# Kernel tuning notes

Measured on AMD Instinct MI355X. Metric: run time of the kernel, lower is better.

## Reference

```python
import jax, jax.numpy as jnp
import numpy as np
import math

L = 4          # n_layers
H = 8          # n_heads
TOP_K = 32
Z99 = 2.326347874040841
SQRT2PI = math.sqrt(2.0 * math.pi)
CONF = 0.99
SCALE_MAX = 1.0  # model not calibrated -> _scale_max = 1.0
EPS = 1e-5


def layer_norm(x, g, b):
    m = jnp.mean(x, axis=-1, keepdims=True)
    v = jnp.var(x, axis=-1, keepdims=True)
    return (x - m) * jax.lax.rsqrt(v + EPS) * g + b


def pos_encoding(T, D):
    pos = jnp.arange(T, dtype=jnp.float32)[:, None]
    div = jnp.exp(jnp.arange(0, D, 2, dtype=jnp.float32) * (-math.log(10000.0) / D))
    pe = jnp.zeros((T, D), jnp.float32)
    pe = pe.at[:, 0::2].set(jnp.sin(pos * div))
    pe = pe.at[:, 1::2].set(jnp.cos(pos * div))
    return pe  # [T, D]


def sparse_attn(h, Wq, Wk, Wv, Wo, bo):
    B, T, D = h.shape
    dh = D // H
    q = (h @ Wq).reshape(B, T, H, dh)
    k = (h @ Wk).reshape(B, T, H, dh)
    v = (h @ Wv).reshape(B, T, H, dh)
    scores = jnp.einsum('bthd,bshd->bhts', q, k) / np.float32(np.sqrt(dh))  # [B,H,T,T]
    kth = jax.lax.top_k(scores, TOP_K)[0][..., -1:]  # k-th largest per row
    scores = jnp.where(scores < kth, -jnp.inf, scores)
    attn = jax.nn.softmax(scores, axis=-1)
    attn = jnp.nan_to_num(attn)
    out = jnp.einsum('bhts,bshd->bthd', attn, v).reshape(B, T, D)
    return out @ Wo + bo


def encoder_layer(h, Wq, Wk, Wv, Wo, bo, W1, b1, W2, b2, g1, be1, g2, be2):
    h = layer_norm(h + sparse_attn(h, Wq, Wk, Wv, Wo, bo), g1, be1)
    ff = jax.nn.gelu((h @ W1) + b1, approximate=False) @ W2 + b2
    return layer_norm(h + ff, g2, be2)


def setup_inputs() -> dict:
    key = jax.random.key(0)
    B, T, Din, D, Dff = 16, 1024, 64, 512, 2048
    ks = jax.random.split(key, 12)

    def p(k, shape):
        return jax.random.normal(k, shape, jnp.float32) * np.float32(1.0 / np.sqrt(shape[-2]))

    return {
        'x': jax.random.normal(ks[0], (B, T, Din), jnp.float32),
        'W_in': p(ks[1], (Din, D)), 'b_in': jnp.zeros((D,), jnp.float32),
        'Wq': p(ks[2], (L, D, D)), 'Wk': p(ks[3], (L, D, D)),
        'Wv': p(ks[4], (L, D, D)), 'Wo': p(ks[5], (L, D, D)),
        'bo': jnp.zeros((L, D), jnp.float32),
        'W1': p(ks[6], (L, D, Dff)), 'b1': jnp.zeros((L, Dff), jnp.float32),
        'W2': p(ks[7], (L, Dff, D)), 'b2': jnp.zeros((L, D), jnp.float32),
        'g1': jnp.ones((L, D), jnp.float32), 'be1': jnp.zeros((L, D), jnp.float32),
        'g2': jnp.ones((L, D), jnp.float32), 'be2': jnp.zeros((L, D), jnp.float32),
        'gm': jnp.ones((D,), jnp.float32), 'bm': jnp.zeros((D,), jnp.float32),
        'Wm': p(ks[8], (D, 1)), 'cm': jnp.zeros((1,), jnp.float32),
        'gs': jnp.ones((D,), jnp.float32), 'bs': jnp.zeros((D,), jnp.float32),
        'Ws': p(ks[9], (D, 1)), 'cs': jnp.zeros((1,), jnp.float32),
    }


def reference(x, W_in, b_in, Wq, Wk, Wv, Wo, bo, W1, b1, W2, b2, g1, be1, g2, be2,
              gm, bm, Wm, cm, gs, bs, Ws, cs):
    B, T, _ = x.shape
    D = W_in.shape[1]
    h = (x @ W_in) + b_in + pos_encoding(T, D)[None]  # input_proj + pos enc (dropout=eval)
    for i in range(L):
        h = encoder_layer(h, Wq[i], Wk[i], Wv[i], Wo[i], bo[i],
                          W1[i], b1[i], W2[i], b2[i], g1[i], be1[i], g2[i], be2[i])
    h_last = h[:, -1, :]  # [B, D]
    mu = (layer_norm(h_last, gm, bm) @ Wm + cm)[:, 0]
    scale = jax.nn.sigmoid(layer_norm(h_last, gs, bs) @ Ws + cs)[:, 0] * SCALE_MAX
    var_pred = mu + scale * Z99
    phi_z = math.exp(-0.5 * Z99 ** 2) / SQRT2PI
    es_pred = mu + scale * phi_z / (1.0 - CONF)
    return jnp.stack([mu, scale, var_pred, es_pred])  # [4, B]
```

## Files before the change

### kernel.cpp

```cpp
#include <hip/hip_runtime.h>
#include <math.h>


typedef unsigned int u32;
typedef __attribute__((ext_vector_type(8))) _Float16 f16x8;
typedef __attribute__((ext_vector_type(4))) float f32x4;

__device__ __forceinline__ void g2l16(const void* g, void* l) {
  __builtin_amdgcn_global_load_lds(
      (const __attribute__((address_space(1))) u32*)g,
      (__attribute__((address_space(3))) u32*)l, 16, 0, 0);
}

__global__ __launch_bounds__(256) void wprep_kernel(const float* __restrict__ src,
    unsigned short* __restrict__ dst_hi, unsigned short* __restrict__ dst_lo,
    int K, int N) {
  __shared__ float t[64][65];
  src    += (size_t)blockIdx.z * K * N;
  dst_hi += (size_t)blockIdx.z * K * N;
  dst_lo += (size_t)blockIdx.z * K * N;
  const int k0 = blockIdx.y * 64, n0 = blockIdx.x * 64;
#pragma unroll
  for (int i = 0; i < 16; i++) {
    int idx = threadIdx.x + i * 256;
    int kk = idx >> 6, nn = idx & 63;
    t[kk][nn] = src[(size_t)(k0 + kk) * N + n0 + nn];
  }
  __syncthreads();
#pragma unroll
  for (int i = 0; i < 16; i++) {
    int idx = threadIdx.x + i * 256;
    int nn = idx >> 6, kk = idx & 63;
    float w = t[kk][nn];
    _Float16 hi = (_Float16)w;
    _Float16 lo = (_Float16)(w - (float)hi);
    union { _Float16 h; unsigned short u; } a, b; a.h = hi; b.h = lo;
    dst_hi[(size_t)(n0 + nn) * K + k0 + kk] = a.u;
    dst_lo[(size_t)(n0 + nn) * K + k0 + kk] = b.u;
  }
}

__global__ __launch_bounds__(256) void gemm_split(const float* __restrict__ A,
    const unsigned short* __restrict__ Bhi, const unsigned short* __restrict__ Blo,
    const float* __restrict__ bias, float* __restrict__ C,
    int M, int N, int K, int ldb, int epi) {
  __shared__ float          As[128 * 64];
  __shared__ unsigned short BsH[128 * 64];
  __shared__ unsigned short BsL[128 * 64];
  const int tid = threadIdx.x;
  const int w = tid >> 6, l = tid & 63;
  const int wm = w >> 1, wn = w & 1;
  const int bm = blockIdx.y * 128, bn = blockIdx.x * 128;
  f32x4 acc[4][4] = {};

  for (int k0 = 0; k0 < K; k0 += 64) {
    if (k0) __syncthreads();
#pragma unroll
    for (int i = 0; i < 8; i++) {
      int cl = i * 256 + w * 64 + l;
      int row = cl >> 4, c = cl & 15;
      int col = (((c >> 1) ^ (row & 7)) * 8) + (c & 1) * 4;
      g2l16(A + (size_t)(bm + row) * K + k0 + col, As + (size_t)(i * 256 + w * 64) * 4);
    }
#pragma unroll
    for (int i = 0; i < 4; i++) {
      int cl = i * 256 + w * 64 + l;
      int row = cl >> 3, c = cl & 7;
      int col = ((c ^ (row & 7)) * 8);
      size_t src = (size_t)(bn + row) * ldb + k0 + col;
      g2l16(Bhi + src, BsH + (size_t)(i * 256 + w * 64) * 8);
      g2l16(Blo + src, BsL + (size_t)(i * 256 + w * 64) * 8);
    }
    __syncthreads();
#pragma unroll
    for (int kk = 0; kk < 2; kk++) {
      f16x8 ahi[4], alo[4], bhi[4], blo[4];
      const int c16 = kk * 4 + (l >> 4);
#pragma unroll
      for (int i = 0; i < 4; i++) {
        int ar = wm * 64 + i * 16 + (l & 15);
        const float* ap = &As[ar * 64 + ((c16 ^ (ar & 7)) * 8)];
        float4 a0 = *(const float4*)ap;
        float4 a1 = *(const float4*)(ap + 4);
        float av[8] = {a0.x, a0.y, a0.z, a0.w, a1.x, a1.y, a1.z, a1.w};
#pragma unroll
        for (int e = 0; e < 8; e++) {
          _Float16 hh = (_Float16)av[e];
          ahi[i][e] = hh;
          alo[i][e] = (_Float16)(av[e] - (float)hh);
        }
        int br = wn * 64 + i * 16 + (l & 15);
        bhi[i] = *(const f16x8*)&BsH[br * 64 + ((c16 ^ (br & 7)) * 8)];
        blo[i] = *(const f16x8*)&BsL[br * 64 + ((c16 ^ (br & 7)) * 8)];
      }
#pragma unroll
      for (int i = 0; i < 4; i++)
#pragma unroll
        for (int j = 0; j < 4; j++) {
          acc[i][j] = __builtin_amdgcn_mfma_f32_16x16x32_f16(ahi[i], bhi[j], acc[i][j], 0, 0, 0);
          acc[i][j] = __builtin_amdgcn_mfma_f32_16x16x32_f16(alo[i], bhi[j], acc[i][j], 0, 0, 0);
          acc[i][j] = __builtin_amdgcn_mfma_f32_16x16x32_f16(ahi[i], blo[j], acc[i][j], 0, 0, 0);
        }
    }
  }

  float bj[4], fr[4];
#pragma unroll
  for (int j = 0; j < 4; j++) {
    int col = bn + wn * 64 + j * 16 + (l & 15);
    bj[j] = (bias != nullptr) ? bias[col] : 0.f;
    fr[j] = (epi == 3) ? __expf((float)(col & ~1) * (-9.210340371976184f / 512.0f)) : 0.f;
  }
#pragma unroll
  for (int i = 0; i < 4; i++) {
#pragma unroll
    for (int e = 0; e < 4; e++) {
      int row = bm + wm * 64 + i * 16 + (l >> 4) * 4 + e;
#pragma unroll
      for (int j = 0; j < 4; j++) {
        int col = bn + wn * 64 + j * 16 + (l & 15);
        float v = acc[i][j][e] + bj[j];
        if (epi == 2) v = 0.5f * v * (1.0f + erff(v * 0.70710678118654752f));
        if (epi == 3) {
          float ang = (float)(row & 1023) * fr[j];
          v += (col & 1) ? cosf(ang) : sinf(ang);
        }
        if (epi == 4) v += C[(size_t)row * N + col];
        C[(size_t)row * N + col] = v;
      }
    }
  }
}

__device__ __forceinline__ unsigned f2o(float f) {
  unsigned b = __float_as_uint(f);
  return (b & 0x80000000u) ? ~b : (b | 0x80000000u);
}
__device__ __forceinline__ float o2f(unsigned u) {
  unsigned b = (u & 0x80000000u) ? (u & 0x7fffffffu) : ~u;
  return __uint_as_float(b);
}

__global__ __launch_bounds__(512, 4) void attn_kernel(float* __restrict__ qa,
    const float* __restrict__ ka, const float* __restrict__ va) {
  __shared__ __align__(16) float smem[16384 + 2048];
  float* ktile = smem;
  float* qlds  = smem + 16384;
  float* cval  = smem;
  int*   cidx  = (int*)smem + 32 * 96;

  const int tid = threadIdx.x;
  const int wave = tid >> 6, lane = tid & 63;
  const int bh = blockIdx.y, b = bh >> 3, hh = bh & 7;
  const int t0 = blockIdx.x * 32;
  const float* kb = ka + (size_t)b * 1024 * 512 + hh * 64;
  const float* vb = va + (size_t)b * 1024 * 512 + hh * 64;

  {
    int row = tid >> 4, qq = tid & 15;
    float4 qv = *(const float4*)(qa + ((size_t)(b * 1024 + t0 + row)) * 512 + hh * 64 + qq * 4);
    qv.x *= 0.125f; qv.y *= 0.125f; qv.z *= 0.125f; qv.w *= 0.125f;
    *(float4*)(qlds + row * 64 + qq * 4) = qv;
  }

  float sc[4][16] = {};

#pragma unroll
  for (int tile = 0; tile < 4; ++tile) {
    const float* kg = kb + (size_t)tile * 256 * 512;
#pragma unroll
    for (int i = 0; i < 8; ++i) {
      int idx = tid + i * 512;
      int row = idx >> 4, qq = idx & 15;
      float4 kv = *(const float4*)(kg + (size_t)row * 512 + qq * 4);
      *(float4*)(ktile + row * 64 + ((qq ^ (row & 7)) * 4)) = kv;
    }
    __syncthreads();
#pragma unroll 4
    for (int dq = 0; dq < 16; ++dq) {
      float4 qr[4];
#pragma unroll
      for (int r = 0; r < 4; ++r)
        qr[r] = *(const float4*)(qlds + (wave * 4 + r) * 64 + dq * 4);
      const int swz = (dq ^ (lane & 7)) * 4;
#pragma unroll
      for (int j = 0; j < 4; ++j) {
        float4 kv = *(const float4*)(ktile + (j * 64 + lane) * 64 + swz);
#pragma unroll
        for (int r = 0; r < 4; ++r) {
          float a = sc[r][tile * 4 + j];
          a = fmaf(qr[r].x, kv.x, a); a = fmaf(qr[r].y, kv.y, a);
          a = fmaf(qr[r].z, kv.z, a); a = fmaf(qr[r].w, kv.w, a);
          sc[r][tile * 4 + j] = a;
        }
      }
    }
    __syncthreads();
  }

  unsigned uu[4][16];
#pragma unroll
  for (int r = 0; r < 4; ++r)
#pragma unroll
    for (int j = 0; j < 16; ++j) uu[r][j] = f2o(sc[r][j]);

#pragma unroll
  for (int r = 0; r < 4; ++r) {
    const int row = wave * 4 + r;
    unsigned m = uu[r][0];
#pragma unroll
    for (int j = 1; j < 16; ++j) m = m > uu[r][j] ? m : uu[r][j];
    unsigned gm = m;
#pragma unroll
    for (int off = 32; off; off >>= 1) {
      unsigned o = __shfl_xor(gm, off);
      gm = gm > o ? gm : o;
    }
    unsigned lam = 0;
    for (int bit = 31; bit >= 16; --bit) {
      unsigned tv = lam | (1u << bit);
      if (__popcll(__ballot(m >= tv)) >= 32) lam = tv;
    }
    int base = 0;
#pragma unroll
    for (int j = 0; j < 16; ++j) {
      bool p = uu[r][j] >= lam;
      unsigned long long mk = __ballot(p);
      int pos = base + (int)__popcll(mk & ((1ull << lane) - 1ull));
      if (p && pos < 96) { cval[row * 96 + pos] = o2f(uu[r][j]); cidx[row * 96 + pos] = j * 64 + lane; }
      base += (int)__popcll(mk);
    }
    int C = base;
    unsigned kth = 0;
    if (C <= 96) {
      unsigned cu0 = (lane < C)      ? f2o(cval[row * 96 + lane])      : 0u;
      unsigned cu1 = (64 + lane < C) ? f2o(cval[row * 96 + 64 + lane]) : 0u;
      for (int bit = 31; bit >= 0; --bit) {
        unsigned tv = kth | (1u << bit);
        int c = (int)__popcll(__ballot(cu0 >= tv)) + (int)__popcll(__ballot(cu1 >= tv));
        if (c >= 32) kth = tv;
      }
    } else {
      for (int bit = 31; bit >= 0; --bit) {
        unsigned tv = kth | (1u << bit);
        int pc = 0;
#pragma unroll
        for (int j = 0; j < 16; ++j) pc += (uu[r][j] >= tv) ? 1 : 0;
#pragma unroll
        for (int off = 32; off; off >>= 1) pc += __shfl_xor(pc, off);
        if (pc >= 32) kth = tv;
      }
      base = 0;
#pragma unroll
      for (int j = 0; j < 16; ++j) {
        bool p = uu[r][j] >= kth;
        unsigned long long mk = __ballot(p);
        int pos = base + (int)__popcll(mk & ((1ull << lane) - 1ull));
        if (p && pos < 96) { cval[row * 96 + pos] = o2f(uu[r][j]); cidx[row * 96 + pos] = j * 64 + lane; }
        base += (int)__popcll(mk);
      }
      C = base < 96 ? base : 96;
    }
    float kth_f = o2f(kth), gm_f = o2f(gm);
    float e0 = 0.f, e1 = 0.f;
    if (lane < C)      { float vv = cval[row * 96 + lane];      if (vv >= kth_f) e0 = __expf(vv - gm_f); }
    if (64 + lane < C) { float vv = cval[row * 96 + 64 + lane]; if (vv >= kth_f) e1 = __expf(vv - gm_f); }
    float ps = e0 + e1;
#pragma unroll
    for (int off = 32; off; off >>= 1) ps += __shfl_xor(ps, off);
    cval[row * 96 + lane] = e0;
    if (lane < 32) cval[row * 96 + 64 + lane] = e1;
    float acc = 0.f;
    for (int i = 0; i < C; ++i) {
      float ev = cval[row * 96 + i];
      int   si = cidx[row * 96 + i];
      acc = fmaf(ev, vb[(size_t)si * 512 + lane], acc);
    }
    qa[((size_t)(b * 1024 + t0 + row)) * 512 + hh * 64 + lane] = acc * (1.f / ps);
  }
}

__global__ __launch_bounds__(256) void resid_ln_kernel(float* __restrict__ h,
    const float* __restrict__ o, const float* __restrict__ g,
    const float* __restrict__ be) {
  const int wave = threadIdx.x >> 6, lane = threadIdx.x & 63;
  const size_t row = (size_t)blockIdx.x * 4 + wave;
  float* hr = h + row * 512;
  const float* orr = o + row * 512;
  float x[8]; float s = 0.f, s2 = 0.f;
#pragma unroll
  for (int j = 0; j < 8; j++) {
    float vv = hr[j * 64 + lane] + orr[j * 64 + lane];
    x[j] = vv; s += vv; s2 += vv * vv;
  }
#pragma unroll
  for (int off = 32; off; off >>= 1) { s += __shfl_xor(s, off); s2 += __shfl_xor(s2, off); }
  float mean = s * (1.f / 512.f);
  float var  = s2 * (1.f / 512.f) - mean * mean;
  float r = rsqrtf(var + 1e-5f);
#pragma unroll
  for (int j = 0; j < 8; j++) {
    int d = j * 64 + lane;
    hr[d] = (x[j] - mean) * r * g[d] + be[d];
  }
}

__global__ __launch_bounds__(256) void head_kernel(const float* __restrict__ h,
    const float* __restrict__ gm, const float* __restrict__ bm,
    const float* __restrict__ Wm, const float* __restrict__ cm,
    const float* __restrict__ gs, const float* __restrict__ bs,
    const float* __restrict__ Ws, const float* __restrict__ cs,
    float* __restrict__ out) {
  const int wave = threadIdx.x >> 6, lane = threadIdx.x & 63;
  const int b = blockIdx.x * 4 + wave;
  const float* hr = h + ((size_t)b * 1024 + 1023) * 512;
  float x[8]; float s = 0.f, s2 = 0.f;
#pragma unroll
  for (int j = 0; j < 8; j++) { float vv = hr[j * 64 + lane]; x[j] = vv; s += vv; s2 += vv * vv; }
#pragma unroll
  for (int off = 32; off; off >>= 1) { s += __shfl_xor(s, off); s2 += __shfl_xor(s2, off); }
  float mean = s * (1.f / 512.f);
  float var  = s2 * (1.f / 512.f) - mean * mean;
  float r = rsqrtf(var + 1e-5f);
  float am = 0.f, as = 0.f;
#pragma unroll
  for (int j = 0; j < 8; j++) {
    int d = j * 64 + lane;
    float n = (x[j] - mean) * r;
    am = fmaf(n * gm[d] + bm[d], Wm[d], am);
    as = fmaf(n * gs[d] + bs[d], Ws[d], as);
  }
#pragma unroll
  for (int off = 32; off; off >>= 1) { am += __shfl_xor(am, off); as += __shfl_xor(as, off); }
  if (lane == 0) {
    const double Z = 2.326347874040841;
    float mu  = am + cm[0];
    float scl = 1.f / (1.f + expf(-(as + cs[0])));
    float esc = (float)(exp(-0.5 * Z * Z) / sqrt(2.0 * 3.14159265358979323846) / 0.01);
    out[b]      = mu;
    out[16 + b] = scl;
    out[32 + b] = mu + scl * (float)Z;
    out[48 + b] = mu + scl * esc;
  }
}

extern "C" void kernel_launch(void* const* d_in, const int* in_sizes, int n_in,
                              void* d_out, int out_size, void* d_ws, size_t ws_size,
                              hipStream_t stream) {
  const float* x    = (const float*)d_in[0];
  const float* W_in = (const float*)d_in[1];
  const float* b_in = (const float*)d_in[2];
  const float* Wq   = (const float*)d_in[3];
  const float* Wk   = (const float*)d_in[4];
  const float* Wv   = (const float*)d_in[5];
  const float* Wo   = (const float*)d_in[6];
  const float* bo   = (const float*)d_in[7];
  const float* W1   = (const float*)d_in[8];
  const float* b1   = (const float*)d_in[9];
  const float* W2   = (const float*)d_in[10];
  const float* b2   = (const float*)d_in[11];
  const float* g1   = (const float*)d_in[12];
  const float* be1  = (const float*)d_in[13];
  const float* g2   = (const float*)d_in[14];
  const float* be2  = (const float*)d_in[15];
  const float* gm   = (const float*)d_in[16];
  const float* bm   = (const float*)d_in[17];
  const float* Wm   = (const float*)d_in[18];
  const float* cm   = (const float*)d_in[19];
  const float* gs   = (const float*)d_in[20];
  const float* bs   = (const float*)d_in[21];
  const float* Ws   = (const float*)d_in[22];
  const float* cs   = (const float*)d_in[23];

  const int M = 16384, D = 512, DFF = 2048;
  float* ws = (float*)d_ws;
  float* h  = ws;
  float* q  = ws +  8388608;
  float* k  = ws + 16777216;
  float* v  = ws + 25165824;
  float* ff = k;
  unsigned short* wb = (unsigned short*)(ws + 33554432);
  unsigned short* WinH = wb;
  unsigned short* WinL = WinH + 32768;
  unsigned short* WqH  = WinL + 32768;
  unsigned short* WqL  = WqH  + 1048576;
  unsigned short* WkH  = WqL  + 1048576;
  unsigned short* WkL  = WkH  + 1048576;
  unsigned short* WvH  = WkL  + 1048576;
  unsigned short* WvL  = WvH  + 1048576;
  unsigned short* WoH  = WvL  + 1048576;
  unsigned short* WoL  = WoH  + 1048576;
  unsigned short* W1H  = WoL  + 1048576;
  unsigned short* W1L  = W1H  + 4194304;
  unsigned short* W2H  = W1L  + 4194304;
  unsigned short* W2L  = W2H  + 4194304;

  dim3 blk(256);

  wprep_kernel<<<dim3(8, 1, 1), blk, 0, stream>>>(W_in, WinH, WinL, 64, 512);
  wprep_kernel<<<dim3(8, 8, 4), blk, 0, stream>>>(Wq, WqH, WqL, 512, 512);
  wprep_kernel<<<dim3(8, 8, 4), blk, 0, stream>>>(Wk, WkH, WkL, 512, 512);
  wprep_kernel<<<dim3(8, 8, 4), blk, 0, stream>>>(Wv, WvH, WvL, 512, 512);
  wprep_kernel<<<dim3(8, 8, 4), blk, 0, stream>>>(Wo, WoH, WoL, 512, 512);
  wprep_kernel<<<dim3(32, 8, 4), blk, 0, stream>>>(W1, W1H, W1L, 512, 2048);
  wprep_kernel<<<dim3(8, 32, 4), blk, 0, stream>>>(W2, W2H, W2L, 2048, 512);

  dim3 gD(4, 128);
  dim3 gH(8, 128);

  gemm_split<<<gD, blk, 0, stream>>>(x, WinH, WinL, b_in, h, M, D, 64, 64, 3);

  for (int l = 0; l < 4; l++) {
    const size_t oD = (size_t)l * D * D;
    const size_t oF = (size_t)l * D * DFF;

    gemm_split<<<gD, blk, 0, stream>>>(h, WqH + oD, WqL + oD, nullptr, q, M, D, D, D, 1);
    gemm_split<<<gD, blk, 0, stream>>>(h, WkH + oD, WkL + oD, nullptr, k, M, D, D, D, 1);
    gemm_split<<<gD, blk, 0, stream>>>(h, WvH + oD, WvL + oD, nullptr, v, M, D, D, D, 1);

    attn_kernel<<<dim3(32, 128), dim3(512), 0, stream>>>(q, k, v);

    gemm_split<<<gD, blk, 0, stream>>>(q, WoH + oD, WoL + oD, bo + (size_t)l * D, k, M, D, D, D, 1);
    resid_ln_kernel<<<dim3(4096), blk, 0, stream>>>(h, k, g1 + (size_t)l * D, be1 + (size_t)l * D);

    gemm_split<<<gH, blk, 0, stream>>>(h, W1H + oF, W1L + oF, b1 + (size_t)l * DFF, ff, M, 1024, D, D, 2);
    gemm_split<<<gD, blk, 0, stream>>>(ff, W2H + oF, W2L + oF, nullptr, q, M, D, 1024, DFF, 1);
    gemm_split<<<gH, blk, 0, stream>>>(h, W1H + oF + 1024 * (size_t)D, W1L + oF + 1024 * (size_t)D,
                                       b1 + (size_t)l * DFF + 1024, ff, M, 1024, D, D, 2);
    gemm_split<<<gD, blk, 0, stream>>>(ff, W2H + oF + 1024, W2L + oF + 1024,
                                       b2 + (size_t)l * D, q, M, D, 1024, DFF, 4);

    resid_ln_kernel<<<dim3(4096), blk, 0, stream>>>(h, q, g2 + (size_t)l * D, be2 + (size_t)l * D);
  }

  head_kernel<<<dim3(4), blk, 0, stream>>>(h, gm, bm, Wm, cm, gs, bs, Ws, cs, (float*)d_out);
}
```

Before: 3.722 ms.

## Compute attention scores with split-fp16 MFMA using head-major Q/K planes

The Q and K projection GEMMs now write their outputs as hi/lo fp16 planes in a per-head, head-major layout. The attention kernel loads these planes into LDS with direct global-to-LDS copies and computes QK^T with three-term split-fp16 MFMA, replacing the scalar FP32 FMA loop. Weight preparation moves into the layer loop, converting one layer at a time into a smaller reused buffer, and attention output goes to a separate buffer. The split-fp16 scores carry slightly different rounding than FP32, which could change which keys fall on the top-k boundary. Scores also pass through an extra LDS transpose with additional barriers.

New measurement: 3.274 ms. 12.0% less time.

```diff
diff --git a/kernel.cpp b/kernel.cpp
--- a/kernel.cpp
+++ b/kernel.cpp
@@ -16,9 +16,6 @@
     unsigned short* __restrict__ dst_hi, unsigned short* __restrict__ dst_lo,
     int K, int N) {
   __shared__ float t[64][65];
-  src    += (size_t)blockIdx.z * K * N;
-  dst_hi += (size_t)blockIdx.z * K * N;
-  dst_lo += (size_t)blockIdx.z * K * N;
   const int k0 = blockIdx.y * 64, n0 = blockIdx.x * 64;
 #pragma unroll
   for (int i = 0; i < 16; i++) {
@@ -43,6 +40,7 @@
 __global__ __launch_bounds__(256) void gemm_split(const float* __restrict__ A,
     const unsigned short* __restrict__ Bhi, const unsigned short* __restrict__ Blo,
     const float* __restrict__ bias, float* __restrict__ C,
+    unsigned short* __restrict__ Ph, unsigned short* __restrict__ Pl,
     int M, int N, int K, int ldb, int epi) {
   __shared__ float          As[128 * 64];
   __shared__ unsigned short BsH[128 * 64];
@@ -102,6 +100,27 @@
           acc[i][j] = __builtin_amdgcn_mfma_f32_16x16x32_f16(ahi[i], blo[j], acc[i][j], 0, 0, 0);
         }
     }
+  }
+
+  if (epi == 5) {
+#pragma unroll
+    for (int i = 0; i < 4; i++)
+#pragma unroll
+      for (int e = 0; e < 4; e++) {
+        int row = bm + wm * 64 + i * 16 + (l >> 4) * 4 + e;
+#pragma unroll
+        for (int j = 0; j < 4; j++) {
+          int col = bn + wn * 64 + j * 16 + (l & 15);
+          float vv = acc[i][j][e];
+          _Float16 hi = (_Float16)vv;
+          _Float16 lo = (_Float16)(vv - (float)hi);
+          union { _Float16 h; unsigned short u; } a, b; a.h = hi; b.h = lo;
+          size_t off = (size_t)(row >> 10) * 524288 + (size_t)(col >> 6) * 65536
+                     + (size_t)(row & 1023) * 64 + (col & 63);
+          Ph[off] = a.u; Pl[off] = b.u;
+        }
+      }
+    return;
   }
 
   float bj[4], fr[4];
@@ -141,59 +160,81 @@
   return __uint_as_float(b);
 }
 
-__global__ __launch_bounds__(512, 4) void attn_kernel(float* __restrict__ qa,
-    const float* __restrict__ ka, const float* __restrict__ va) {
-  __shared__ __align__(16) float smem[16384 + 2048];
-  float* ktile = smem;
-  float* qlds  = smem + 16384;
-  float* cval  = smem;
-  int*   cidx  = (int*)smem + 32 * 96;
+__global__ __launch_bounds__(512, 4) void attn_kernel(
+    const unsigned short* __restrict__ qh, const unsigned short* __restrict__ ql,
+    const unsigned short* __restrict__ kh, const unsigned short* __restrict__ kl,
+    const float* __restrict__ va, float* __restrict__ ao) {
+  __shared__ __align__(16) float smem[14464];
+  unsigned short* Qhs = (unsigned short*)smem;
+  unsigned short* Qls = Qhs + 2048;
+  unsigned short* Khs = Qhs + 4096;
+  unsigned short* Kls = Qhs + 12288;
+  float* S    = smem + 10240;
+  float* cval = smem + 2048;
+  int*   cidx = (int*)smem + 5120;
 
   const int tid = threadIdx.x;
   const int wave = tid >> 6, lane = tid & 63;
   const int bh = blockIdx.y, b = bh >> 3, hh = bh & 7;
   const int t0 = blockIdx.x * 32;
-  const float* kb = ka + (size_t)b * 1024 * 512 + hh * 64;
-  const float* vb = va + (size_t)b * 1024 * 512 + hh * 64;
+  const size_t hoff = (size_t)bh * 65536;
+  const float* vb = va + (size_t)b * 524288 + hh * 64;
 
   {
-    int row = tid >> 4, qq = tid & 15;
-    float4 qv = *(const float4*)(qa + ((size_t)(b * 1024 + t0 + row)) * 512 + hh * 64 + qq * 4);
-    qv.x *= 0.125f; qv.y *= 0.125f; qv.z *= 0.125f; qv.w *= 0.125f;
-    *(float4*)(qlds + row * 64 + qq * 4) = qv;
-  }
-
-  float sc[4][16] = {};
-
-#pragma unroll
-  for (int tile = 0; tile < 4; ++tile) {
-    const float* kg = kb + (size_t)tile * 256 * 512;
-#pragma unroll
-    for (int i = 0; i < 8; ++i) {
-      int idx = tid + i * 512;
-      int row = idx >> 4, qq = idx & 15;
-      float4 kv = *(const float4*)(kg + (size_t)row * 512 + qq * 4);
-      *(float4*)(ktile + row * 64 + ((qq ^ (row & 7)) * 4)) = kv;
+    int plane = tid >> 8, cl = tid & 255;
+    int row = cl >> 3, c = cl & 7;
+    size_t src = hoff + (size_t)(t0 + row) * 64 + ((c ^ (row & 7)) * 8);
+    g2l16((plane ? ql : qh) + src, (plane ? Qls : Qhs) + cl * 8);
+  }
+
+  float sc[4][16];
+
+  for (int kt = 0; kt < 8; ++kt) {
+#pragma unroll
+    for (int i = 0; i < 2; ++i) {
+      int cl = tid + i * 512;
+      int row = cl >> 3, c = cl & 7;
+      size_t src = hoff + (size_t)(kt * 128 + row) * 64 + ((c ^ (row & 7)) * 8);
+      g2l16(kh + src, Khs + cl * 8);
+      g2l16(kl + src, Kls + cl * 8);
     }
     __syncthreads();
-#pragma unroll 4
-    for (int dq = 0; dq < 16; ++dq) {
-      float4 qr[4];
-#pragma unroll
-      for (int r = 0; r < 4; ++r)
-        qr[r] = *(const float4*)(qlds + (wave * 4 + r) * 64 + dq * 4);
-      const int swz = (dq ^ (lane & 7)) * 4;
-#pragma unroll
-      for (int j = 0; j < 4; ++j) {
-        float4 kv = *(const float4*)(ktile + (j * 64 + lane) * 64 + swz);
-#pragma unroll
-        for (int r = 0; r < 4; ++r) {
-          float a = sc[r][tile * 4 + j];
-          a = fmaf(qr[r].x, kv.x, a); a = fmaf(qr[r].y, kv.y, a);
-          a = fmaf(qr[r].z, kv.z, a); a = fmaf(qr[r].w, kv.w, a);
-          sc[r][tile * 4 + j] = a;
-        }
-      }
+
+    f32x4 a0 = {}, a1 = {};
+#pragma unroll
+    for (int ks = 0; ks < 2; ++ks) {
+      int c = (lane >> 4) + ks * 4;
+      int kr = wave * 16 + (lane & 15);
+      int ko = kr * 64 + ((c ^ (kr & 7)) * 8);
+      f16x8 kfh = *(const f16x8*)&Khs[ko];
+      f16x8 kfl = *(const f16x8*)&Kls[ko];
+      int q0 = lane & 15;
+      int o0 = q0 * 64 + ((c ^ (q0 & 7)) * 8);
+      f16x8 qf0h = *(const f16x8*)&Qhs[o0];
+      f16x8 qf0l = *(const f16x8*)&Qls[o0];
+      int q1 = 16 + (lane & 15);
+      int o1 = q1 * 64 + ((c ^ (q1 & 7)) * 8);
+      f16x8 qf1h = *(const f16x8*)&Qhs[o1];
+      f16x8 qf1l = *(const f16x8*)&Qls[o1];
+      a0 = __builtin_amdgcn_mfma_f32_16x16x32_f16(kfh, qf0h, a0, 0, 0, 0);
+      a0 = __builtin_amdgcn_mfma_f32_16x16x32_f16(kfl, qf0h, a0, 0, 0, 0);
+      a0 = __builtin_amdgcn_mfma_f32_16x16x32_f16(kfh, qf0l, a0, 0, 0, 0);
+      a1 = __builtin_amdgcn_mfma_f32_16x16x32_f16(kfh, qf1h, a1, 0, 0, 0);
+      a1 = __builtin_amdgcn_mfma_f32_16x16x32_f16(kfl, qf1h, a1, 0, 0, 0);
+      a1 = __builtin_amdgcn_mfma_f32_16x16x32_f16(kfh, qf1l, a1, 0, 0, 0);
+    }
+#pragma unroll
+    for (int e = 0; e < 4; ++e) {
+      int srow = wave * 16 + (lane >> 4) * 4 + e;
+      S[srow * 33 + (lane & 15)]      = a0[e];
+      S[srow * 33 + 16 + (lane & 15)] = a1[e];
+    }
+    __syncthreads();
+#pragma unroll
+    for (int r = 0; r < 4; ++r) {
+      int qr = wave * 4 + r;
+      sc[r][kt * 2]     = S[lane * 33 + qr] * 0.125f;
+      sc[r][kt * 2 + 1] = S[(64 + lane) * 33 + qr] * 0.125f;
     }
     __syncthreads();
   }
@@ -276,7 +317,7 @@
       int   si = cidx[row * 96 + i];
       acc = fmaf(ev, vb[(size_t)si * 512 + lane], acc);
     }
-    qa[((size_t)(b * 1024 + t0 + row)) * 512 + hh * 64 + lane] = acc * (1.f / ps);
+    ao[((size_t)(b * 1024 + t0 + row)) * 512 + hh * 64 + lane] = acc * (1.f / ps);
   }
 }
 
@@ -374,63 +415,63 @@
 
   const int M = 16384, D = 512, DFF = 2048;
   float* ws = (float*)d_ws;
-  float* h  = ws;
-  float* q  = ws +  8388608;
-  float* k  = ws + 16777216;
-  float* v  = ws + 25165824;
-  float* ff = k;
-  unsigned short* wb = (unsigned short*)(ws + 33554432);
-  unsigned short* WinH = wb;
+  float* h   = ws;
+  unsigned short* qhp = (unsigned short*)(ws + 8388608);
+  unsigned short* qlp = qhp + 8388608;
+  unsigned short* khp = (unsigned short*)(ws + 16777216);
+  unsigned short* klp = khp + 8388608;
+  float* v   = ws + 25165824;
+  float* ao  = ws + 33554432;
+  float* ff  = ws + 8388608;
+  unsigned short* wl = (unsigned short*)(ws + 41943040);
+  unsigned short* WqH = wl,            *WqL = wl + 262144;
+  unsigned short* WkH = wl + 524288,   *WkL = wl + 786432;
+  unsigned short* WvH = wl + 1048576,  *WvL = wl + 1310720;
+  unsigned short* WoH = wl + 1572864,  *WoL = wl + 1835008;
+  unsigned short* W1H = wl + 2097152,  *W1L = wl + 3145728;
+  unsigned short* W2H = wl + 4194304,  *W2L = wl + 5242880;
+  unsigned short* WinH = (unsigned short*)(ws + 45088768);
   unsigned short* WinL = WinH + 32768;
-  unsigned short* WqH  = WinL + 32768;
-  unsigned short* WqL  = WqH  + 1048576;
-  unsigned short* WkH  = WqL  + 1048576;
-  unsigned short* WkL  = WkH  + 1048576;
-  unsigned short* WvH  = WkL  + 1048576;
-  unsigned short* WvL  = WvH  + 1048576;
-  unsigned short* WoH  = WvL  + 1048576;
-  unsigned short* WoL  = WoH  + 1048576;
-  unsigned short* W1H  = WoL  + 1048576;
-  unsigned short* W1L  = W1H  + 4194304;
-  unsigned short* W2H  = W1L  + 4194304;
-  unsigned short* W2L  = W2H  + 4194304;
 
   dim3 blk(256);
-
-  wprep_kernel<<<dim3(8, 1, 1), blk, 0, stream>>>(W_in, WinH, WinL, 64, 512);
-  wprep_kernel<<<dim3(8, 8, 4), blk, 0, stream>>>(Wq, WqH, WqL, 512, 512);
-  wprep_kernel<<<dim3(8, 8, 4), blk, 0, stream>>>(Wk, WkH, WkL, 512, 512);
-  wprep_kernel<<<dim3(8, 8, 4), blk, 0, stream>>>(Wv, WvH, WvL, 512, 512);
-  wprep_kernel<<<dim3(8, 8, 4), blk, 0, stream>>>(Wo, WoH, WoL, 512, 512);
-  wprep_kernel<<<dim3(32, 8, 4), blk, 0, stream>>>(W1, W1H, W1L, 512, 2048);
-  wprep_kernel<<<dim3(8, 32, 4), blk, 0, stream>>>(W2, W2H, W2L, 2048, 512);
-
   dim3 gD(4, 128);
   dim3 gH(8, 128);
 
-  gemm_split<<<gD, blk, 0, stream>>>(x, WinH, WinL, b_in, h, M, D, 64, 64, 3);
+  wprep_kernel<<<dim3(8, 1, 1), blk, 0, stream>>>(W_in, WinH, WinL, 64, 512);
+  gemm_split<<<gD, blk, 0, stream>>>(x, WinH, WinL, b_in, h, nullptr, nullptr, M, D, 64, 64, 3);
 
   for (int l = 0; l < 4; l++) {
-    const size_t oD = (size_t)l * D * D;
-    const size_t oF = (size_t)l * D * DFF;
-
-    gemm_split<<<gD, blk, 0, stream>>>(h, WqH + oD, WqL + oD, nullptr, q, M, D, D, D, 1);
-    gemm_split<<<gD, blk, 0, stream>>>(h, WkH + oD, WkL + oD, nullptr, k, M, D, D, D, 1);
-    gemm_split<<<gD, blk, 0, stream>>>(h, WvH + oD, WvL + oD, nullptr, v, M, D, D, D, 1);
-
-    attn_kernel<<<dim3(32, 128), dim3(512), 0, stream>>>(q, k, v);
-
-    gemm_split<<<gD, blk, 0, stream>>>(q, WoH + oD, WoL + oD, bo + (size_t)l * D, k, M, D, D, D, 1);
-    resid_ln_kernel<<<dim3(4096), blk, 0, stream>>>(h, k, g1 + (size_t)l * D, be1 + (size_t)l * D);
-
-    gemm_split<<<gH, blk, 0, stream>>>(h, W1H + oF, W1L + oF, b1 + (size_t)l * DFF, ff, M, 1024, D, D, 2);
-    gemm_split<<<gD, blk, 0, stream>>>(ff, W2H + oF, W2L + oF, nullptr, q, M, D, 1024, DFF, 1);
-    gemm_split<<<gH, blk, 0, stream>>>(h, W1H + oF + 1024 * (size_t)D, W1L + oF + 1024 * (size_t)D,
-                                       b1 + (size_t)l * DFF + 1024, ff, M, 1024, D, D, 2);
-    gemm_split<<<gD, blk, 0, stream>>>(ff, W2H + oF + 1024, W2L + oF + 1024,
-                                       b2 + (size_t)l * D, q, M, D, 1024, DFF, 4);
-
-    resid_ln_kernel<<<dim3(4096), blk, 0, stream>>>(h, q, g2 + (size_t)l * D, be2 + (size_t)l * D);
+    const float* wq = Wq + (size_t)l * 262144;
+    const float* wk = Wk + (size_t)l * 262144;
+    const float* wv = Wv + (size_t)l * 262144;
+    const float* wo = Wo + (size_t)l * 262144;
+    const float* w1 = W1 + (size_t)l * 1048576;
+    const float* w2 = W2 + (size_t)l * 1048576;
+
+    wprep_kernel<<<dim3(8, 8, 1), blk, 0, stream>>>(wq, WqH, WqL, 512, 512);
+    wprep_kernel<<<dim3(8, 8, 1), blk, 0, stream>>>(wk, WkH, WkL, 512, 512);
+    wprep_kernel<<<dim3(8, 8, 1), blk, 0, stream>>>(wv, WvH, WvL, 512, 512);
+    wprep_kernel<<<dim3(8, 8, 1), blk, 0, stream>>>(wo, WoH, WoL, 512, 512);
+    wprep_kernel<<<dim3(32, 8, 1), blk, 0, stream>>>(w1, W1H, W1L, 512, 2048);
+    wprep_kernel<<<dim3(8, 32, 1), blk, 0, stream>>>(w2, W2H, W2L, 2048, 512);
+
+    gemm_split<<<gD, blk, 0, stream>>>(h, WqH, WqL, nullptr, nullptr, qhp, qlp, M, D, D, D, 5);
+    gemm_split<<<gD, blk, 0, stream>>>(h, WkH, WkL, nullptr, nullptr, khp, klp, M, D, D, D, 5);
+    gemm_split<<<gD, blk, 0, stream>>>(h, WvH, WvL, nullptr, v, nullptr, nullptr, M, D, D, D, 1);
+
+    attn_kernel<<<dim3(32, 128), dim3(512), 0, stream>>>(qhp, qlp, khp, klp, v, ao);
+
+    gemm_split<<<gD, blk, 0, stream>>>(ao, WoH, WoL, bo + (size_t)l * D, v, nullptr, nullptr, M, D, D, D, 1);
+    resid_ln_kernel<<<dim3(4096), blk, 0, stream>>>(h, v, g1 + (size_t)l * D, be1 + (size_t)l * D);
+
+    gemm_split<<<gH, blk, 0, stream>>>(h, W1H, W1L, b1 + (size_t)l * DFF, ff, nullptr, nullptr, M, 1024, D, D, 2);
+    gemm_split<<<gD, blk, 0, stream>>>(ff, W2H, W2L, nullptr, ao, nullptr, nullptr, M, D, 1024, DFF, 1);
+    gemm_split<<<gH, blk, 0, stream>>>(h, W1H + 524288, W1L + 524288,
+                                       b1 + (size_t)l * DFF + 1024, ff, nullptr, nullptr, M, 1024, D, D, 2);
+    gemm_split<<<gD, blk, 0, stream>>>(ff, W2H + 1024, W2L + 1024,
+                                       b2 + (size_t)l * D, ao, nullptr, nullptr, M, D, 1024, DFF, 4);
+
+    resid_ln_kernel<<<dim3(4096), blk, 0, stream>>>(h, ao, g2 + (size_t)l * D, be2 + (size_t)l * D);
   }
 
   head_kernel<<<dim3(4), blk, 0, stream>>>(h, gm, bm, Wm, cm, gs, bs, Ws, cs, (float*)d_out);
```
